# Performance work log

Hardware: AMD Instinct MI355X
Metric: run time of the kernel (lower is better)

## Reference

```python
import jax, jax.numpy as jnp
import numpy as np

E, K, H, I = 8, 2, 1024, 3584  # num_experts, top_k, hidden, intermediate


def setup_inputs() -> dict:
    key = jax.random.key(0)
    k0, k1, k2, k3, k4 = jax.random.split(key, 5)
    scale = 0.02
    return {
        "hidden_states": jax.random.normal(k0, (2, 1024, H), dtype=jnp.float32),
        "w_gate": jax.random.normal(k1, (E, H), dtype=jnp.float32) * scale,  # gate Linear H->E
        "w1": jax.random.normal(k2, (E, I, H), dtype=jnp.float32) * scale,   # gate proj
        "w3": jax.random.normal(k3, (E, I, H), dtype=jnp.float32) * scale,   # up proj
        "w2": jax.random.normal(k4, (E, H, I), dtype=jnp.float32) * scale,   # down proj
    }


def reference(hidden_states, w_gate, w1, w3, w2):
    B, S, Hd = hidden_states.shape
    x = hidden_states.reshape(-1, Hd)                       # [T, H]
    logits = jnp.einsum('th,eh->te', x, w_gate)             # router logits [T, E]
    probs = jax.nn.softmax(logits, axis=-1)
    topw, topi = jax.lax.top_k(probs, K)                    # [T, K]
    topw = topw / jnp.sum(topw, axis=-1, keepdims=True)     # renormalize=True
    # dense combine weights [T, E] (zero off the top-k)
    comb = jnp.sum(jax.nn.one_hot(topi, E, dtype=x.dtype) * topw[..., None], axis=1)
    # SwiGLU experts (dense reference over all experts; math matches dispatch+combine)
    g = jnp.einsum('th,eih->eti', x, w1)                    # [E, T, I]
    u = jnp.einsum('th,eih->eti', x, w3)
    h = jax.nn.silu(g) * u
    out = jnp.einsum('eti,ehi->eth', h, w2)                 # [E, T, H]
    y = jnp.einsum('te,eth->th', comb, out)                 # weighted combine
    return y.reshape(B, S, Hd)
```

## Files before the change

### kernel.cpp

```cpp
#include <hip/hip_runtime.h>
#include <hip/hip_bf16.h>
#include <stdint.h>

#define NEXP 8
#define HD 1024
#define ID 3584
#define NTOK 2048
#define NSLOT 4096
#define SLOT_PAD 128
#define NSLOT_ALLOC (NSLOT + SLOT_PAD)
#define WN (NEXP * ID * HD)
#define KSPLIT 4
#define KLEN (ID / KSPLIT)

typedef unsigned short u16;
typedef __attribute__((ext_vector_type(8))) short s16x8;
typedef __attribute__((ext_vector_type(4))) short s16x4;
typedef __attribute__((ext_vector_type(4))) float f32x4;

__device__ __forceinline__ u16 f2bf(float f) {
    __hip_bfloat16 h = __float2bfloat16(f);
    union { __hip_bfloat16 h; u16 u; } v; v.h = h; return v.u;
}

__device__ __forceinline__ s16x8 cvt8(f32x4 a, f32x4 b) {
    s16x8 o;
    o[0]=(short)f2bf(a[0]); o[1]=(short)f2bf(a[1]); o[2]=(short)f2bf(a[2]); o[3]=(short)f2bf(a[3]);
    o[4]=(short)f2bf(b[0]); o[5]=(short)f2bf(b[1]); o[6]=(short)f2bf(b[2]); o[7]=(short)f2bf(b[3]);
    return o;
}

__device__ __forceinline__ void glds16(const void* g, void* l) {
    __builtin_amdgcn_global_load_lds((const __attribute__((address_space(1))) unsigned*)g,
                                     (__attribute__((address_space(3))) unsigned*)l, 16, 0, 0);
}

__global__ void init_kernel(int* __restrict__ counts) {
    if (threadIdx.x < 16) counts[threadIdx.x] = 0;
}

__global__ void router_kernel(const float* __restrict__ x, const float* __restrict__ wg,
                              int* __restrict__ topk_idx, float* __restrict__ topk_w,
                              int* __restrict__ counts) {
    int t = blockIdx.x;
    int lane = threadIdx.x;
    const float* xr = x + (size_t)t * HD;
    float acc[NEXP];
#pragma unroll
    for (int e = 0; e < NEXP; ++e) acc[e] = 0.f;
#pragma unroll
    for (int i = 0; i < HD / 256; ++i) {
        int h = i * 256 + lane * 4;
        f32x4 xv = *(const f32x4*)(xr + h);
#pragma unroll
        for (int e = 0; e < NEXP; ++e) {
            f32x4 wv = *(const f32x4*)(wg + e * HD + h);
            acc[e] += xv[0]*wv[0] + xv[1]*wv[1] + xv[2]*wv[2] + xv[3]*wv[3];
        }
    }
#pragma unroll
    for (int e = 0; e < NEXP; ++e) {
#pragma unroll
        for (int s = 32; s > 0; s >>= 1) acc[e] += __shfl_xor(acc[e], s, 64);
    }
    if (lane == 0) {
        int b0 = 0; float l0 = acc[0];
#pragma unroll
        for (int e = 1; e < NEXP; ++e) if (acc[e] > l0) { l0 = acc[e]; b0 = e; }
        int b1 = (b0 == 0) ? 1 : 0; float l1 = acc[b1];
#pragma unroll
        for (int e = 0; e < NEXP; ++e) {
            if (e == b0 || e == b1) continue;
            if (acc[e] > l1) { l1 = acc[e]; b1 = e; }
        }
        float w0 = 1.f / (1.f + expf(l1 - l0));
        float w1 = 1.f - w0;
        topk_idx[2 * t] = b0; topk_idx[2 * t + 1] = b1;
        topk_w[2 * t] = w0;  topk_w[2 * t + 1] = w1;
        atomicAdd(&counts[b0], 1);
        atomicAdd(&counts[b1], 1);
    }
}

__global__ void scan_kernel(const int* __restrict__ counts, int* __restrict__ offsets,
                            int* __restrict__ rows) {
    if (threadIdx.x == 0) {
        int off = 0;
#pragma unroll
        for (int e = 0; e < NEXP; ++e) { offsets[e] = off; off += counts[e]; }
    }
    if (threadIdx.x < SLOT_PAD) rows[NSLOT + threadIdx.x] = 0;
}

__global__ void assign_kernel(const int* __restrict__ topk_idx, const int* __restrict__ offsets,
                              int* __restrict__ counts2, int* __restrict__ rows,
                              int* __restrict__ slot_of) {
    int i = blockIdx.x * 256 + threadIdx.x;
    int e = topk_idx[i];
    int pos = atomicAdd(&counts2[e], 1);
    int slot = offsets[e] + pos;
    rows[slot] = i >> 1;
    slot_of[i] = slot;
}

__global__ __launch_bounds__(256)
void cvt3_kernel(const float* __restrict__ x, u16* __restrict__ xbf,
                 const float* __restrict__ w1, u16* __restrict__ w1bf,
                 const float* __restrict__ w3, u16* __restrict__ w3bf) {
    const int NX = NTOK * HD / 8, NW = WN / 8;
    int stride = gridDim.x * 256;
    for (int i = blockIdx.x * 256 + threadIdx.x; i < NX + 2 * NW; i += stride) {
        const float* s; u16* d; int j;
        if (i < NX)            { s = x;  d = xbf;  j = i; }
        else if (i < NX + NW)  { s = w1; d = w1bf; j = i - NX; }
        else                   { s = w3; d = w3bf; j = i - NX - NW; }
        f32x4 v0 = ((const f32x4*)s)[2 * j];
        f32x4 v1 = ((const f32x4*)s)[2 * j + 1];
        ((s16x8*)d)[j] = cvt8(v0, v1);
    }
}

#define G1_BLOCKS (NEXP * (NTOK / 128) * (ID / 128))
#define CVT2_BLOCKS 1024
__global__ __launch_bounds__(512, 4)
void gemm1_kernel(const u16* __restrict__ xbf, const u16* __restrict__ w1bf,
                  const u16* __restrict__ w3bf, const int* __restrict__ counts,
                  const int* __restrict__ offsets, const int* __restrict__ rows,
                  u16* __restrict__ hbuf,
                  const float* __restrict__ w2, u16* __restrict__ w2bf) {
    __shared__ u16 As[128][32];
    __shared__ u16 B1s[128][32];
    __shared__ u16 B3s[128][32];

    if (blockIdx.x >= G1_BLOCKS) {
        const int stride = CVT2_BLOCKS * 512;
        for (int i = (blockIdx.x - G1_BLOCKS) * 512 + threadIdx.x; i < WN / 8; i += stride) {
            f32x4 v0 = ((const f32x4*)w2)[2 * i];
            f32x4 v1 = ((const f32x4*)w2)[2 * i + 1];
            ((s16x8*)w2bf)[i] = cvt8(v0, v1);
        }
        return;
    }

    int bid = blockIdx.x;
    int gq = bid >> 7;
    int rm = bid & 127;
    int mt = rm >> 3;
    int g  = gq * 8 + (rm & 7);
    int e  = g / 28;
    int nt = g - e * 28;

    int n_e = counts[e];
    int m0 = mt * 128;
    if (m0 >= n_e) return;
    int off = offsets[e];
    int n0 = nt * 128;

    int tid = threadIdx.x;
    int lane = tid & 63;
    int wid = tid >> 6;

    int srow = wid * 16 + (lane >> 2);
    int chunk = ((lane & 3) ^ ((srow >> 1) & 3)) * 8;

    int tokA = rows[off + m0 + srow];
    const u16* srcA  = xbf + (size_t)tokA * HD + chunk;
    const u16* srcB1 = w1bf + ((size_t)e * ID + n0 + srow) * HD + chunk;
    const u16* srcB3 = w3bf + ((size_t)e * ID + n0 + srow) * HD + chunk;

    f32x4 accg[4][2] = {}, accu[4][2] = {};
    int wm = (wid >> 2) * 64;
    int wn = (wid & 3) * 32;
    int lr = lane & 15;
    int k8sw = ((lane >> 4) ^ ((lr >> 1) & 3)) * 8;

    for (int k0 = 0; k0 < HD; k0 += 32) {
        glds16(srcA + k0,  &As[wid * 16][0]);
        glds16(srcB1 + k0, &B1s[wid * 16][0]);
        glds16(srcB3 + k0, &B3s[wid * 16][0]);
        __syncthreads();
        s16x8 a[4], b1[2], b3[2];
#pragma unroll
        for (int f = 0; f < 4; ++f)
            a[f] = *(const s16x8*)&As[wm + f * 16 + lr][k8sw];
#pragma unroll
        for (int f = 0; f < 2; ++f) {
            b1[f] = *(const s16x8*)&B1s[wn + f * 16 + lr][k8sw];
            b3[f] = *(const s16x8*)&B3s[wn + f * 16 + lr][k8sw];
        }
#pragma unroll
        for (int fm = 0; fm < 4; ++fm)
#pragma unroll
            for (int fn = 0; fn < 2; ++fn) {
                accg[fm][fn] = __builtin_amdgcn_mfma_f32_16x16x32_bf16(a[fm], b1[fn], accg[fm][fn], 0, 0, 0);
                accu[fm][fn] = __builtin_amdgcn_mfma_f32_16x16x32_bf16(a[fm], b3[fn], accu[fm][fn], 0, 0, 0);
            }
        __syncthreads();
    }

    int lc = lane & 15;
    int lr4 = (lane >> 4) * 4;
#pragma unroll
    for (int fm = 0; fm < 4; ++fm) {
#pragma unroll
        for (int r = 0; r < 4; ++r) {
            int row = wm + fm * 16 + lr4 + r;
            if (m0 + row < n_e) {
                size_t base = (size_t)(off + m0 + row) * ID + n0 + wn;
#pragma unroll
                for (int fn = 0; fn < 2; ++fn) {
                    float g2 = accg[fm][fn][r];
                    float u = accu[fm][fn][r];
                    float hv = g2 * u / (1.f + expf(-g2));
                    hbuf[base + fn * 16 + lc] = f2bf(hv);
                }
            }
        }
    }
}

__global__ __launch_bounds__(512, 4)
void gemm2_kernel(const u16* __restrict__ hbuf, const u16* __restrict__ w2bf,
                  const int* __restrict__ counts, const int* __restrict__ offsets,
                  float* __restrict__ out2) {
    int bid = blockIdx.x;
    int e = bid & 7;
    int inner = bid >> 3;
    int mt = inner >> 5;
    int r2 = inner & 31;
    int nt = r2 >> 2;
    int ks = r2 & 3;

    int n_e = counts[e];
    int m0 = mt * 128;
    if (m0 >= n_e) return;
    int off = offsets[e];
    int n0 = nt * 128;
    int kbase = ks * KLEN;

    __shared__ u16 As[128][32];
    __shared__ u16 Bs[128][32];

    int tid = threadIdx.x;
    int lane = tid & 63;
    int wid = tid >> 6;

    int srow = wid * 16 + (lane >> 2);
    int chunk = ((lane & 3) ^ ((srow >> 1) & 3)) * 8;
    const u16* srcA = hbuf + (size_t)(off + m0 + srow) * ID + kbase + chunk;
    const u16* srcB = w2bf + ((size_t)e * HD + n0 + srow) * ID + kbase + chunk;

    f32x4 acc[4][2] = {};
    int wm = (wid >> 2) * 64;
    int wn = (wid & 3) * 32;
    int lr = lane & 15;
    int k8sw = ((lane >> 4) ^ ((lr >> 1) & 3)) * 8;

    for (int k0 = 0; k0 < KLEN; k0 += 32) {
        glds16(srcA + k0, &As[wid * 16][0]);
        glds16(srcB + k0, &Bs[wid * 16][0]);
        __syncthreads();
        s16x8 a[4], b[2];
#pragma unroll
        for (int f = 0; f < 4; ++f)
            a[f] = *(const s16x8*)&As[wm + f * 16 + lr][k8sw];
#pragma unroll
        for (int f = 0; f < 2; ++f)
            b[f] = *(const s16x8*)&Bs[wn + f * 16 + lr][k8sw];
#pragma unroll
        for (int fm = 0; fm < 4; ++fm)
#pragma unroll
            for (int fn = 0; fn < 2; ++fn)
                acc[fm][fn] = __builtin_amdgcn_mfma_f32_16x16x32_bf16(a[fm], b[fn], acc[fm][fn], 0, 0, 0);
        __syncthreads();
    }

    float* outp = out2 + (size_t)ks * NSLOT_ALLOC * HD;
    int lc = lane & 15;
    int lr4 = (lane >> 4) * 4;
#pragma unroll
    for (int fm = 0; fm < 4; ++fm) {
#pragma unroll
        for (int r = 0; r < 4; ++r) {
            int row = wm + fm * 16 + lr4 + r;
            if (m0 + row < n_e) {
                float* dst = outp + (size_t)(off + m0 + row) * HD + n0 + wn;
#pragma unroll
                for (int fn = 0; fn < 2; ++fn)
                    dst[fn * 16 + lc] = acc[fm][fn][r];
            }
        }
    }
}

__global__ void combine_kernel(const float* __restrict__ out2, const int* __restrict__ slot_of,
                               const float* __restrict__ topk_w, float* __restrict__ y) {
    int i = blockIdx.x * 256 + threadIdx.x;
    int t = i >> 8;
    int c = i & 255;
    int s0 = slot_of[2 * t], s1 = slot_of[2 * t + 1];
    float w0 = topk_w[2 * t], w1 = topk_w[2 * t + 1];
    f32x4 o = {0.f, 0.f, 0.f, 0.f};
#pragma unroll
    for (int ks = 0; ks < KSPLIT; ++ks) {
        const float* p = out2 + (size_t)ks * NSLOT_ALLOC * HD;
        f32x4 a = ((const f32x4*)(p + (size_t)s0 * HD))[c];
        f32x4 b = ((const f32x4*)(p + (size_t)s1 * HD))[c];
#pragma unroll
        for (int j = 0; j < 4; ++j) o[j] += w0 * a[j] + w1 * b[j];
    }
    ((f32x4*)(y + (size_t)t * HD))[c] = o;
}

extern "C" void kernel_launch(void* const* d_in, const int* in_sizes, int n_in,
                              void* d_out, int out_size, void* d_ws, size_t ws_size,
                              hipStream_t stream) {
    (void)in_sizes; (void)n_in; (void)out_size; (void)ws_size;
    const float* x  = (const float*)d_in[0];
    const float* wg = (const float*)d_in[1];
    const float* w1 = (const float*)d_in[2];
    const float* w3 = (const float*)d_in[3];
    const float* w2 = (const float*)d_in[4];
    float* y = (float*)d_out;

    char* ws = (char*)d_ws;
    int*   counts   = (int*)(ws + 0);
    int*   counts2  = (int*)(ws + 32);
    int*   offsets  = (int*)(ws + 64);
    int*   topk_idx = (int*)(ws + 128);
    float* topk_w   = (float*)(ws + 128 + (size_t)NSLOT * 4);
    int*   rows     = (int*)(ws + 128 + (size_t)NSLOT * 8);
    int*   slot_of  = (int*)(ws + 128 + (size_t)NSLOT * 8 + (size_t)NSLOT_ALLOC * 4);
    size_t off_xbf = 128 + (size_t)NSLOT * 12 + (size_t)NSLOT_ALLOC * 4;
    off_xbf = (off_xbf + 255) & ~(size_t)255;
    u16* xbf = (u16*)(ws + off_xbf);
    size_t off_h = off_xbf + (size_t)NTOK * HD * 2;
    u16* hbuf = (u16*)(ws + off_h);
    size_t off_w1 = off_h + (size_t)NSLOT_ALLOC * ID * 2;
    u16* w1bf = (u16*)(ws + off_w1);
    size_t off_w3 = off_w1 + (size_t)WN * 2;
    u16* w3bf = (u16*)(ws + off_w3);
    size_t off_w2 = off_w3 + (size_t)WN * 2;
    u16* w2bf = (u16*)(ws + off_w2);
    size_t off_o2 = off_w2 + (size_t)WN * 2;
    float* out2 = (float*)(ws + off_o2);

    init_kernel<<<1, 64, 0, stream>>>(counts);
    router_kernel<<<NTOK, 64, 0, stream>>>(x, wg, topk_idx, topk_w, counts);
    scan_kernel<<<1, 128, 0, stream>>>(counts, offsets, rows);
    assign_kernel<<<NSLOT / 256, 256, 0, stream>>>(topk_idx, offsets, counts2, rows, slot_of);
    cvt3_kernel<<<4096, 256, 0, stream>>>(x, xbf, w1, w1bf, w3, w3bf);
    gemm1_kernel<<<G1_BLOCKS + CVT2_BLOCKS, 512, 0, stream>>>(xbf, w1bf, w3bf, counts, offsets, rows, hbuf, w2, w2bf);
    gemm2_kernel<<<NEXP * (NTOK / 128) * (HD / 128) * KSPLIT, 512, 0, stream>>>(hbuf, w2bf, counts, offsets, out2);
    combine_kernel<<<(NTOK * HD / 4) / 256, 256, 0, stream>>>(out2, slot_of, topk_w, y);
}
```

Baseline: 344.8 us.

## Enlarge gemm1 tile to 256 rows with double-buffered LDS and phased MFMA scheduling

Reworks the gate/up GEMM to use 256x128 tiles with a K-step of 64 and double-buffered shared memory. The global-to-LDS loads for the next K tile are interleaved between four MFMA phases, using explicit barriers, waitcnt and setprio. The larger tile gives more reuse of each loaded row and overlaps memory traffic with compute, at the cost of more registers and LDS and lower occupancy (launch bounds 2). Slot padding and the scan block size are raised to cover the larger row tile.

```diff
diff --git a/kernel.cpp b/kernel.cpp
--- a/kernel.cpp
+++ b/kernel.cpp
@@ -7,7 +7,7 @@
 #define ID 3584
 #define NTOK 2048
 #define NSLOT 4096
-#define SLOT_PAD 128
+#define SLOT_PAD 256
 #define NSLOT_ALLOC (NSLOT + SLOT_PAD)
 #define WN (NEXP * ID * HD)
 #define KSPLIT 4
@@ -17,6 +17,11 @@
 typedef __attribute__((ext_vector_type(8))) short s16x8;
 typedef __attribute__((ext_vector_type(4))) short s16x4;
 typedef __attribute__((ext_vector_type(4))) float f32x4;
+
+#define BARRIER() __builtin_amdgcn_s_barrier()
+#define LGKM0()   asm volatile("s_waitcnt lgkmcnt(0)" ::: "memory")
+#define VMCNT0()  asm volatile("s_waitcnt vmcnt(0)" ::: "memory")
+#define SCHEDB()  __builtin_amdgcn_sched_barrier(0)
 
 __device__ __forceinline__ u16 f2bf(float f) {
     __hip_bfloat16 h = __float2bfloat16(f);
@@ -120,17 +125,17 @@
     }
 }
 
-#define G1_BLOCKS (NEXP * (NTOK / 128) * (ID / 128))
+#define G1_BLOCKS (NEXP * (NTOK / 256) * (ID / 128))
 #define CVT2_BLOCKS 1024
-__global__ __launch_bounds__(512, 4)
+__global__ __launch_bounds__(512, 2)
 void gemm1_kernel(const u16* __restrict__ xbf, const u16* __restrict__ w1bf,
                   const u16* __restrict__ w3bf, const int* __restrict__ counts,
                   const int* __restrict__ offsets, const int* __restrict__ rows,
                   u16* __restrict__ hbuf,
                   const float* __restrict__ w2, u16* __restrict__ w2bf) {
-    __shared__ u16 As[128][32];
-    __shared__ u16 B1s[128][32];
-    __shared__ u16 B3s[128][32];
+    __shared__ u16 As[2][256][64];
+    __shared__ u16 B1s[2][128][64];
+    __shared__ u16 B3s[2][128][64];
 
     if (blockIdx.x >= G1_BLOCKS) {
         const int stride = CVT2_BLOCKS * 512;
@@ -143,15 +148,15 @@
     }
 
     int bid = blockIdx.x;
-    int gq = bid >> 7;
-    int rm = bid & 127;
+    int q = bid >> 6;
+    int rm = bid & 63;
     int mt = rm >> 3;
-    int g  = gq * 8 + (rm & 7);
+    int g  = q * 8 + (rm & 7);
     int e  = g / 28;
     int nt = g - e * 28;
 
     int n_e = counts[e];
-    int m0 = mt * 128;
+    int m0 = mt * 256;
     if (m0 >= n_e) return;
     int off = offsets[e];
     int n0 = nt * 128;
@@ -160,48 +165,123 @@
     int lane = tid & 63;
     int wid = tid >> 6;
 
-    int srow = wid * 16 + (lane >> 2);
-    int chunk = ((lane & 3) ^ ((srow >> 1) & 3)) * 8;
-
-    int tokA = rows[off + m0 + srow];
-    const u16* srcA  = xbf + (size_t)tokA * HD + chunk;
-    const u16* srcB1 = w1bf + ((size_t)e * ID + n0 + srow) * HD + chunk;
-    const u16* srcB3 = w3bf + ((size_t)e * ID + n0 + srow) * HD + chunk;
-
-    f32x4 accg[4][2] = {}, accu[4][2] = {};
-    int wm = (wid >> 2) * 64;
+    int rsub = lane >> 3;
+    int srcg = ((lane & 7) ^ rsub) * 8;
+
+    const u16* srcA[4];
+#pragma unroll
+    for (int qq = 0; qq < 4; ++qq) {
+        int rl = qq * 64 + wid * 8 + rsub;
+        int tok = rows[off + m0 + rl];
+        srcA[qq] = xbf + (size_t)tok * HD + srcg;
+    }
+    const u16 *srcB1[2], *srcB3[2];
+#pragma unroll
+    for (int qq = 0; qq < 2; ++qq) {
+        int rl = qq * 64 + wid * 8 + rsub;
+        srcB1[qq] = w1bf + ((size_t)e * ID + n0 + rl) * HD + srcg;
+        srcB3[qq] = w3bf + ((size_t)e * ID + n0 + rl) * HD + srcg;
+    }
+
+    f32x4 accg[8][2] = {}, accu[8][2] = {};
+    int wm = (wid >> 2) * 128;
     int wn = (wid & 3) * 32;
     int lr = lane & 15;
-    int k8sw = ((lane >> 4) ^ ((lr >> 1) & 3)) * 8;
-
-    for (int k0 = 0; k0 < HD; k0 += 32) {
-        glds16(srcA + k0,  &As[wid * 16][0]);
-        glds16(srcB1 + k0, &B1s[wid * 16][0]);
-        glds16(srcB3 + k0, &B3s[wid * 16][0]);
-        __syncthreads();
-        s16x8 a[4], b1[2], b3[2];
-#pragma unroll
-        for (int f = 0; f < 4; ++f)
-            a[f] = *(const s16x8*)&As[wm + f * 16 + lr][k8sw];
-#pragma unroll
-        for (int f = 0; f < 2; ++f) {
-            b1[f] = *(const s16x8*)&B1s[wn + f * 16 + lr][k8sw];
-            b3[f] = *(const s16x8*)&B3s[wn + f * 16 + lr][k8sw];
-        }
-#pragma unroll
-        for (int fm = 0; fm < 4; ++fm)
-#pragma unroll
-            for (int fn = 0; fn < 2; ++fn) {
-                accg[fm][fn] = __builtin_amdgcn_mfma_f32_16x16x32_bf16(a[fm], b1[fn], accg[fm][fn], 0, 0, 0);
-                accu[fm][fn] = __builtin_amdgcn_mfma_f32_16x16x32_bf16(a[fm], b3[fn], accu[fm][fn], 0, 0, 0);
-            }
-        __syncthreads();
+    int kk = lane >> 4;
+    int ks0 = ((kk)     ^ (lr & 7)) * 8;
+    int ks1 = ((4 + kk) ^ (lr & 7)) * 8;
+
+#pragma unroll
+    for (int qq = 0; qq < 4; ++qq) glds16(srcA[qq], &As[0][qq * 64 + wid * 8][0]);
+#pragma unroll
+    for (int qq = 0; qq < 2; ++qq) {
+        glds16(srcB1[qq], &B1s[0][qq * 64 + wid * 8][0]);
+        glds16(srcB3[qq], &B3s[0][qq * 64 + wid * 8][0]);
+    }
+    VMCNT0();
+    BARRIER();
+
+    const int NKT = HD / 64;
+    s16x8 a0[8], a1[8], bfr[2];
+    for (int kt = 0; kt < NKT; ++kt) {
+        int cur = kt & 1, nxt = cur ^ 1;
+        bool more = (kt + 1) < NKT;
+        int nk = (kt + 1) * 64;
+
+#pragma unroll
+        for (int f = 0; f < 8; ++f) a0[f] = *(const s16x8*)&As[cur][wm + f * 16 + lr][ks0];
+#pragma unroll
+        for (int fn = 0; fn < 2; ++fn) bfr[fn] = *(const s16x8*)&B1s[cur][wn + fn * 16 + lr][ks0];
+        if (more) {
+            glds16(srcA[0] + nk, &As[nxt][0 * 64 + wid * 8][0]);
+            glds16(srcA[1] + nk, &As[nxt][1 * 64 + wid * 8][0]);
+        }
+        BARRIER(); LGKM0(); SCHEDB();
+        __builtin_amdgcn_s_setprio(1);
+#pragma unroll
+        for (int f = 0; f < 8; ++f)
+#pragma unroll
+            for (int fn = 0; fn < 2; ++fn)
+                accg[f][fn] = __builtin_amdgcn_mfma_f32_16x16x32_bf16(a0[f], bfr[fn], accg[f][fn], 0, 0, 0);
+        __builtin_amdgcn_s_setprio(0);
+        BARRIER();
+
+#pragma unroll
+        for (int fn = 0; fn < 2; ++fn) bfr[fn] = *(const s16x8*)&B3s[cur][wn + fn * 16 + lr][ks0];
+        if (more) {
+            glds16(srcA[2] + nk, &As[nxt][2 * 64 + wid * 8][0]);
+            glds16(srcA[3] + nk, &As[nxt][3 * 64 + wid * 8][0]);
+        }
+        BARRIER(); LGKM0(); SCHEDB();
+        __builtin_amdgcn_s_setprio(1);
+#pragma unroll
+        for (int f = 0; f < 8; ++f)
+#pragma unroll
+            for (int fn = 0; fn < 2; ++fn)
+                accu[f][fn] = __builtin_amdgcn_mfma_f32_16x16x32_bf16(a0[f], bfr[fn], accu[f][fn], 0, 0, 0);
+        __builtin_amdgcn_s_setprio(0);
+        BARRIER();
+
+#pragma unroll
+        for (int f = 0; f < 8; ++f) a1[f] = *(const s16x8*)&As[cur][wm + f * 16 + lr][ks1];
+#pragma unroll
+        for (int fn = 0; fn < 2; ++fn) bfr[fn] = *(const s16x8*)&B1s[cur][wn + fn * 16 + lr][ks1];
+        if (more) {
+            glds16(srcB1[0] + nk, &B1s[nxt][0 * 64 + wid * 8][0]);
+            glds16(srcB1[1] + nk, &B1s[nxt][1 * 64 + wid * 8][0]);
+        }
+        BARRIER(); LGKM0(); SCHEDB();
+        __builtin_amdgcn_s_setprio(1);
+#pragma unroll
+        for (int f = 0; f < 8; ++f)
+#pragma unroll
+            for (int fn = 0; fn < 2; ++fn)
+                accg[f][fn] = __builtin_amdgcn_mfma_f32_16x16x32_bf16(a1[f], bfr[fn], accg[f][fn], 0, 0, 0);
+        __builtin_amdgcn_s_setprio(0);
+        BARRIER();
+
+#pragma unroll
+        for (int fn = 0; fn < 2; ++fn) bfr[fn] = *(const s16x8*)&B3s[cur][wn + fn * 16 + lr][ks1];
+        if (more) {
+            glds16(srcB3[0] + nk, &B3s[nxt][0 * 64 + wid * 8][0]);
+            glds16(srcB3[1] + nk, &B3s[nxt][1 * 64 + wid * 8][0]);
+        }
+        BARRIER(); LGKM0(); SCHEDB();
+        __builtin_amdgcn_s_setprio(1);
+#pragma unroll
+        for (int f = 0; f < 8; ++f)
+#pragma unroll
+            for (int fn = 0; fn < 2; ++fn)
+                accu[f][fn] = __builtin_amdgcn_mfma_f32_16x16x32_bf16(a1[f], bfr[fn], accu[f][fn], 0, 0, 0);
+        __builtin_amdgcn_s_setprio(0);
+        VMCNT0();
+        BARRIER();
     }
 
     int lc = lane & 15;
     int lr4 = (lane >> 4) * 4;
 #pragma unroll
-    for (int fm = 0; fm < 4; ++fm) {
+    for (int fm = 0; fm < 8; ++fm) {
 #pragma unroll
         for (int r = 0; r < 4; ++r) {
             int row = wm + fm * 16 + lr4 + r;
@@ -347,7 +427,7 @@
 
     init_kernel<<<1, 64, 0, stream>>>(counts);
     router_kernel<<<NTOK, 64, 0, stream>>>(x, wg, topk_idx, topk_w, counts);
-    scan_kernel<<<1, 128, 0, stream>>>(counts, offsets, rows);
+    scan_kernel<<<1, 256, 0, stream>>>(counts, offsets, rows);
     assign_kernel<<<NSLOT / 256, 256, 0, stream>>>(topk_idx, offsets, counts2, rows, slot_of);
     cvt3_kernel<<<4096, 256, 0, stream>>>(x, xbf, w1, w1bf, w3, w3bf);
     gemm1_kernel<<<G1_BLOCKS + CVT2_BLOCKS, 512, 0, stream>>>(xbf, w1bf, w3bf, counts, offsets, rows, hbuf, w2, w2bf);
```

Result: slower. 386.4 us (+12.1%).
